# Kernel tuning notes

Measured on AMD Instinct MI355X. Metric: run time of the kernel, lower is better.

## Reference

```python
import jax, jax.numpy as jnp
import numpy as np

N, E, D, H, C, ED = 30000, 300000, 256, 8, 32, 32
HID = H * C  # 256 = hidden_channels


def setup_inputs() -> dict:
    key = jax.random.key(0)
    ks = jax.random.split(key, 14)
    w = lambda k, shp, fan: (jax.random.normal(k, shp, jnp.float32) / np.sqrt(fan)).astype(jnp.float32)
    return {
        "x": jax.random.normal(ks[0], (N, D), jnp.float32),
        "edge_index": jax.random.randint(ks[1], (2, E), 0, N, jnp.int32),
        "edge_attr": jax.random.normal(ks[2], (E, ED), jnp.float32),
        # TransformerConv params (PyG: q/k/v Linears have bias; lin_edge & lin_skip bias=False)
        "Wq": w(ks[3], (D, HID), D), "bq": 0.01 * jax.random.normal(ks[4], (HID,), jnp.float32),
        "Wk": w(ks[5], (D, HID), D), "bk": 0.01 * jax.random.normal(ks[6], (HID,), jnp.float32),
        "Wv": w(ks[7], (D, HID), D), "bv": 0.01 * jax.random.normal(ks[8], (HID,), jnp.float32),
        "We": w(ks[9], (ED, HID), ED),
        "Wskip": w(ks[10], (D, HID), D),
        # MLP([HID, HID, HID], gelu-tanh, plain_last=False): two Linear+act layers
        "W1": w(ks[11], (HID, HID), HID), "b1": jnp.zeros((HID,), jnp.float32),
        "W2": w(ks[12], (HID, HID), HID), "b2": jnp.zeros((HID,), jnp.float32),
    }


def reference(x, edge_index, edge_attr, Wq, bq, Wk, bk, Wv, bv, We, Wskip, W1, b1, W2, b2):
    src, dst = edge_index[0], edge_index[1]  # message flows src -> dst
    q = (x @ Wq + bq).reshape(N, H, C)
    k = (x @ Wk + bk).reshape(N, H, C)
    v = (x @ Wv + bv).reshape(N, H, C)
    e = (edge_attr @ We).reshape(E, H, C)
    k_e = k[src] + e                               # [E,H,C]
    v_e = v[src] + e                               # [E,H,C]
    logits = jnp.einsum('ehc,ehc->eh', q[dst], k_e) / np.sqrt(C)  # [E,H]
    # segment softmax over incoming edges of each dst node
    m = jax.ops.segment_max(logits, dst, num_segments=N)          # [N,H]
    a = jnp.exp(logits - m[dst])
    denom = jax.ops.segment_sum(a, dst, num_segments=N)           # [N,H]
    alpha = a / (denom[dst] + 1e-16)                              # [E,H]
    agg = jax.ops.segment_sum(alpha[:, :, None] * v_e, dst, num_segments=N)  # [N,H,C]
    out = agg.reshape(N, HID) + x @ Wskip          # concat heads + root skip
    # residual MLP: x + gelu(gelu(x W1 + b1) W2 + b2)
    h = jax.nn.gelu(out @ W1 + b1, approximate=True)
    h = jax.nn.gelu(h @ W2 + b2, approximate=True)
    return out + h
```

## Files before the change

### kernel.cpp

```cpp
#include <hip/hip_runtime.h>

#define NN 30000
#define NE 300000
#define HIDDEN 256

typedef __attribute__((ext_vector_type(8))) __bf16 bf16x8;
typedef __attribute__((ext_vector_type(4))) __bf16 bf16x4;
typedef __attribute__((ext_vector_type(4))) float float4v;

__device__ inline __bf16 f2bf(float f) {
  unsigned u = __builtin_bit_cast(unsigned, f);
  u += 0x7fffu + ((u >> 16) & 1u);
  unsigned short s = (unsigned short)(u >> 16);
  return __builtin_bit_cast(__bf16, s);
}
__device__ inline float bf2f(__bf16 b) {
  unsigned short s = __builtin_bit_cast(unsigned short, b);
  unsigned u = ((unsigned)s) << 16;
  return __builtin_bit_cast(float, u);
}
__device__ inline float gelu_tanh(float x) {
  float x3 = x * x * x;
  return 0.5f * x * (1.0f + tanhf(0.79788456080286536f * (x + 0.044715f * x3)));
}

#define PREP_XB_END (1829 + (NN * 32 + 255) / 256)
__global__ __launch_bounds__(256) void prep_kernel(
    const float* __restrict__ Wq, const float* __restrict__ Wk, const float* __restrict__ Wv,
    const float* __restrict__ Wsk, const float* __restrict__ W1, const float* __restrict__ W2,
    const float* __restrict__ We, const float* __restrict__ bq, const float* __restrict__ bk,
    const float* __restrict__ bv, const float* __restrict__ x,
    __bf16* __restrict__ WTall, __bf16* __restrict__ WT1, __bf16* __restrict__ WT2,
    float* __restrict__ ball, float* __restrict__ WeT, __bf16* __restrict__ xb,
    int* __restrict__ degz) {
  const int b = blockIdx.x;
  const int tid = threadIdx.x;
  if (b < 1792) {
    const int region = b >> 8;
    const int idx = ((b & 255) << 8) | tid;
    const int k = idx & 255, n = idx >> 8;
    float v;
    if (region == 3) {
      const int h = n >> 5, d = n & 31;
      const float* wq = Wq + (size_t)k * 256 + h * 32;
      const float* we = We + (size_t)d * 256 + h * 32;
      float s = 0.f;
#pragma unroll
      for (int c = 0; c < 32; ++c) s += wq[c] * we[c];
      v = s;
    } else {
      const float* W = (region == 0) ? Wq : (region == 1) ? Wk : (region == 2) ? Wv
                     : (region == 4) ? Wsk : (region == 5) ? W1 : W2;
      v = W[(size_t)k * 256 + n];
    }
    const __bf16 bv16 = f2bf(v);
    if (region < 5) WTall[(size_t)region * 65536 + idx] = bv16;
    else if (region == 5) WT1[idx] = bv16;
    else WT2[idx] = bv16;
  } else if (b < 1797) {
    const int j = (b - 1792) * 256 + tid;
    if (j < 1280) {
      float v = 0.f;
      if (j < 256) v = bq[j];
      else if (j < 512) v = bk[j - 256];
      else if (j < 768) v = bv[j - 512];
      else if (j < 1024) {
        const int col = j - 768, h = col >> 5, d = col & 31;
        const float* bqh = bq + h * 32;
        const float* we = We + (size_t)d * 256 + h * 32;
        float s = 0.f;
#pragma unroll
        for (int c = 0; c < 32; ++c) s += bqh[c] * we[c];
        v = s;
      }
      ball[j] = v;
    }
  } else if (b < 1829) {
    const int idx = (b - 1797) * 256 + tid;
    const int ch = idx >> 5, d = idx & 31;
    WeT[idx] = We[(size_t)d * 256 + ch];
  } else if (b < PREP_XB_END) {
    const int t = (b - 1829) * 256 + tid;
    if (t < NN * 256 / 8) {
      const float* p = x + (size_t)t * 8;
      float4v f0 = *(const float4v*)(p);
      float4v f1 = *(const float4v*)(p + 4);
      bf16x8 o;
#pragma unroll
      for (int j = 0; j < 4; ++j) { o[j] = f2bf(f0[j]); o[j + 4] = f2bf(f1[j]); }
      *(bf16x8*)(xb + (size_t)t * 8) = o;
    }
  } else {
    const int idx = (b - PREP_XB_END) * 256 + tid;
    if (idx < 2 * NN) degz[idx] = 0;
  }
}

__global__ void count_deg_kernel(const int* __restrict__ dst, int* __restrict__ deg, int E) {
  int e = blockIdx.x * 256 + threadIdx.x;
  if (e < E) atomicAdd(&deg[dst[e]], 1);
}

__global__ __launch_bounds__(256) void deg_psum_kernel(const int* __restrict__ deg,
                                                       int* __restrict__ psum, int n) {
  int i = blockIdx.x * 256 + threadIdx.x;
  int v = (i < n) ? deg[i] : 0;
#pragma unroll
  for (int s = 1; s < 64; s <<= 1) v += __shfl_xor(v, s);
  __shared__ int ws[4];
  if ((threadIdx.x & 63) == 0) ws[threadIdx.x >> 6] = v;
  __syncthreads();
  if (threadIdx.x == 0) psum[blockIdx.x] = ws[0] + ws[1] + ws[2] + ws[3];
}

__global__ __launch_bounds__(128) void psum_scan_kernel(int* __restrict__ psum,
                                                        int* __restrict__ offs, int nb) {
  __shared__ int tmp[128];
  const int t = threadIdx.x;
  int v = (t < nb) ? psum[t] : 0;
  tmp[t] = v;
  __syncthreads();
  for (int s = 1; s < 128; s <<= 1) {
    int u = (t >= s) ? tmp[t - s] : 0;
    __syncthreads();
    tmp[t] += u;
    __syncthreads();
  }
  if (t < nb) psum[t] = tmp[t] - v;
  if (t == 0) offs[NN] = NE;
}

__global__ __launch_bounds__(256) void offs_kernel(const int* __restrict__ deg,
                                                   const int* __restrict__ psum,
                                                   int* __restrict__ offs, int n) {
  __shared__ int tmp[256];
  const int t = threadIdx.x;
  const int i = blockIdx.x * 256 + t;
  int v = (i < n) ? deg[i] : 0;
  tmp[t] = v;
  __syncthreads();
  for (int s = 1; s < 256; s <<= 1) {
    int u = (t >= s) ? tmp[t - s] : 0;
    __syncthreads();
    tmp[t] += u;
    __syncthreads();
  }
  if (i < n) offs[i] = psum[blockIdx.x] + tmp[t] - v;
}

__global__ void scatter_kernel(const int* __restrict__ srcIn, const int* __restrict__ dstIn,
                               const float* __restrict__ ea,
                               const int* __restrict__ offs, int* __restrict__ cursor,
                               int* __restrict__ srcs, __bf16* __restrict__ eaC, int E) {
  int e = blockIdx.x * 256 + threadIdx.x;
  if (e >= E) return;
  const float* src = ea + (size_t)e * 32;
  float4v f[8];
#pragma unroll
  for (int t = 0; t < 8; ++t) f[t] = *(const float4v*)(src + t * 4);
  int d = dstIn[e];
  int p = atomicAdd(&cursor[d], 1);
  int o = offs[d] + p;
  srcs[o] = srcIn[e];
  __bf16* dstp = eaC + (size_t)o * 32;
#pragma unroll
  for (int t = 0; t < 4; ++t) {
    bf16x8 b;
#pragma unroll
    for (int j = 0; j < 4; ++j) { b[j] = f2bf(f[t * 2][j]); b[j + 4] = f2bf(f[t * 2 + 1][j]); }
    *(bf16x8*)(dstp + t * 8) = b;
  }
}

template <int GX, int EPI, int MODE>
__global__ __launch_bounds__(256) void gemm_k4(
    const __bf16* __restrict__ A, const __bf16* __restrict__ Wt,
    const float* __restrict__ bias,
    float* __restrict__ Yf, __bf16* __restrict__ Ybf,
    __bf16* __restrict__ QGp, __bf16* __restrict__ KVp,
    const float* __restrict__ resid, int M, int gyTiles) {
  __shared__ char smem[128 * 264 * 2];
  __bf16* Bs = (__bf16*)smem;
  const int bid = blockIdx.x;
  const int stripe = bid / (8 * GX);
  const int rem = bid % (8 * GX);
  const int y8 = rem % 8;
  const int xt = rem / 8;
  const int y = stripe * 8 + y8;
  if (y >= gyTiles) return;
  const int n0 = xt * 128;

  {
    const int t = threadIdx.x;
#pragma unroll
    for (int i = 0; i < 16; ++i) {
      int g = i * 256 + t;
      int row = g >> 5;
      int c16 = g & 31;
      bf16x8 v = *(const bf16x8*)(Wt + (size_t)(n0 + row) * 256 + c16 * 8);
      *(bf16x8*)(Bs + row * 264 + c16 * 8) = v;
    }
  }
  __syncthreads();

  const int lane = threadIdx.x & 63;
  const int w = threadIdx.x >> 6;
  const int r = lane & 15;
  const int q = lane >> 4;
  const int mw = y * 128 + w * 32;
  int ar0 = mw + r;      if (ar0 >= M) ar0 = M - 1;
  int ar1 = mw + 16 + r; if (ar1 >= M) ar1 = M - 1;
  const int kq = q * 8;

  float4v acc[2][8];
#pragma unroll
  for (int i = 0; i < 2; ++i)
#pragma unroll
    for (int t = 0; t < 8; ++t) acc[i][t] = (float4v){0.f, 0.f, 0.f, 0.f};

#pragma unroll
  for (int kk = 0; kk < 256; kk += 32) {
    const int ka = kk + kq;
    bf16x8 a0 = *(const bf16x8*)(A + (size_t)ar0 * 256 + ka);
    bf16x8 a1 = *(const bf16x8*)(A + (size_t)ar1 * 256 + ka);
    bf16x8 b[8];
#pragma unroll
    for (int t = 0; t < 8; ++t)
      b[t] = *(const bf16x8*)(Bs + (t * 16 + r) * 264 + ka);
#pragma unroll
    for (int t = 0; t < 8; ++t) {
      acc[0][t] = __builtin_amdgcn_mfma_f32_16x16x32_bf16(a0, b[t], acc[0][t], 0, 0, 0);
      acc[1][t] = __builtin_amdgcn_mfma_f32_16x16x32_bf16(a1, b[t], acc[1][t], 0, 0, 0);
    }
  }
  __syncthreads();

  float* cs = (float*)smem + w * 4224;
#pragma unroll
  for (int t = 0; t < 8; ++t) {
    const int col = n0 + t * 16 + r;
    const float bb = bias ? bias[col] : 0.0f;
#pragma unroll
    for (int i2 = 0; i2 < 2; ++i2)
#pragma unroll
      for (int ii = 0; ii < 4; ++ii) {
        float v = acc[i2][t][ii] + bb;
        if constexpr (EPI == 2 || EPI == 3) v = gelu_tanh(v);
        cs[(i2 * 16 + q * 4 + ii) * 132 + t * 16 + r] = v;
      }
  }

  constexpr int NSTR = GX * 128;
  const int p = n0 >> 8;
  const int cbase = n0 & 255;
  __bf16* dstI = (p == 0 || p == 3) ? QGp : KVp;
  const int moff = (p >= 2) ? 4 : 0;
#pragma unroll
  for (int i = 0; i < 16; ++i) {
    const int rl = i * 2 + (lane >> 5);
    const int row = mw + rl;
    const int c4 = (lane & 31) * 4;
    float4v v = *(const float4v*)(cs + rl * 132 + c4);
    if (row < M) {
      if constexpr (MODE == 1) {
        if (p == 4) {
          *(float4v*)(Yf + (size_t)row * 256 + cbase + c4) = v;
        } else {
          bf16x4 b4;
          b4[0] = f2bf(v[0]); b4[1] = f2bf(v[1]); b4[2] = f2bf(v[2]); b4[3] = f2bf(v[3]);
          const int c = cbase + c4;
          *(bf16x4*)(dstI + (size_t)row * 512 + 2 * c + moff) = b4;
        }
      } else if constexpr (EPI == 1) {
        *(float4v*)(Yf + (size_t)row * NSTR + n0 + c4) = v;
      } else if constexpr (EPI == 3) {
        float4v rr = *(const float4v*)(resid + (size_t)row * NSTR + n0 + c4);
        v[0] += rr[0]; v[1] += rr[1]; v[2] += rr[2]; v[3] += rr[3];
        *(float4v*)(Yf + (size_t)row * NSTR + n0 + c4) = v;
      } else {
        bf16x4 b4;
        b4[0] = f2bf(v[0]); b4[1] = f2bf(v[1]); b4[2] = f2bf(v[2]); b4[3] = f2bf(v[3]);
        *(bf16x4*)(Ybf + (size_t)row * NSTR + n0 + c4) = b4;
      }
    }
  }
}

__global__ __launch_bounds__(256) void attn_kernel(
    const __bf16* __restrict__ QG, const __bf16* __restrict__ KV,
    const __bf16* __restrict__ eaC,
    const int* __restrict__ srcs, const int* __restrict__ offs,
    float* __restrict__ OUT, __bf16* __restrict__ AE) {
  __shared__ float sdn[4][64];
  __shared__ float sav[4][64][4], sae[4][64][4];
  const int lane = threadIdx.x & 63;
  const int w = threadIdx.x >> 6;
  const int n = blockIdx.x;
  const int sub = lane & 7;

  const float LSC = 0.25506589858f;
  const bf16x8 qg = *(const bf16x8*)(QG + (size_t)n * 512 + lane * 8);
  const float q0 = bf2f(qg[0]) * LSC, q1 = bf2f(qg[1]) * LSC;
  const float q2 = bf2f(qg[2]) * LSC, q3 = bf2f(qg[3]) * LSC;
  const float g0 = bf2f(qg[4]) * LSC, g1 = bf2f(qg[5]) * LSC;
  const float g2 = bf2f(qg[6]) * LSC, g3 = bf2f(qg[7]) * LSC;

  float denom = 0.f;
  float4v accv = {0.f, 0.f, 0.f, 0.f};
  float4v acce = {0.f, 0.f, 0.f, 0.f};
  const int beg = offs[n], end = offs[n + 1];

  int i = beg + w;
  for (; i + 4 < end; i += 8) {
    const int s0 = srcs[i];
    const int s1 = srcs[i + 4];
    const bf16x8 kv0 = *(const bf16x8*)(KV + (size_t)s0 * 512 + lane * 8);
    const bf16x4 a0 = *(const bf16x4*)(eaC + (size_t)i * 32 + sub * 4);
    const bf16x8 kv1 = *(const bf16x8*)(KV + (size_t)s1 * 512 + lane * 8);
    const bf16x4 a1 = *(const bf16x4*)(eaC + (size_t)(i + 4) * 32 + sub * 4);
    const float e00 = bf2f(a0[0]), e01 = bf2f(a0[1]), e02 = bf2f(a0[2]), e03 = bf2f(a0[3]);
    const float e10 = bf2f(a1[0]), e11 = bf2f(a1[1]), e12 = bf2f(a1[2]), e13 = bf2f(a1[3]);
    float p0 = q0 * bf2f(kv0[0]) + q1 * bf2f(kv0[1]) + q2 * bf2f(kv0[2]) + q3 * bf2f(kv0[3])
             + g0 * e00 + g1 * e01 + g2 * e02 + g3 * e03;
    float p1 = q0 * bf2f(kv1[0]) + q1 * bf2f(kv1[1]) + q2 * bf2f(kv1[2]) + q3 * bf2f(kv1[3])
             + g0 * e10 + g1 * e11 + g2 * e12 + g3 * e13;
    p0 += __shfl_xor(p0, 1); p1 += __shfl_xor(p1, 1);
    p0 += __shfl_xor(p0, 2); p1 += __shfl_xor(p1, 2);
    p0 += __shfl_xor(p0, 4); p1 += __shfl_xor(p1, 4);
    const float w0 = exp2f(p0);
    const float w1 = exp2f(p1);
    denom += w0 + w1;
    accv[0] += w0 * bf2f(kv0[4]) + w1 * bf2f(kv1[4]);
    accv[1] += w0 * bf2f(kv0[5]) + w1 * bf2f(kv1[5]);
    accv[2] += w0 * bf2f(kv0[6]) + w1 * bf2f(kv1[6]);
    accv[3] += w0 * bf2f(kv0[7]) + w1 * bf2f(kv1[7]);
    acce[0] += w0 * e00 + w1 * e10;
    acce[1] += w0 * e01 + w1 * e11;
    acce[2] += w0 * e02 + w1 * e12;
    acce[3] += w0 * e03 + w1 * e13;
  }
  if (i < end) {
    const int s0 = srcs[i];
    const bf16x8 kv0 = *(const bf16x8*)(KV + (size_t)s0 * 512 + lane * 8);
    const bf16x4 a0 = *(const bf16x4*)(eaC + (size_t)i * 32 + sub * 4);
    const float e00 = bf2f(a0[0]), e01 = bf2f(a0[1]), e02 = bf2f(a0[2]), e03 = bf2f(a0[3]);
    float p0 = q0 * bf2f(kv0[0]) + q1 * bf2f(kv0[1]) + q2 * bf2f(kv0[2]) + q3 * bf2f(kv0[3])
             + g0 * e00 + g1 * e01 + g2 * e02 + g3 * e03;
    p0 += __shfl_xor(p0, 1);
    p0 += __shfl_xor(p0, 2);
    p0 += __shfl_xor(p0, 4);
    const float w0 = exp2f(p0);
    denom += w0;
    accv[0] += w0 * bf2f(kv0[4]);
    accv[1] += w0 * bf2f(kv0[5]);
    accv[2] += w0 * bf2f(kv0[6]);
    accv[3] += w0 * bf2f(kv0[7]);
    acce[0] += w0 * e00;
    acce[1] += w0 * e01;
    acce[2] += w0 * e02;
    acce[3] += w0 * e03;
  }

  sdn[w][lane] = denom;
#pragma unroll
  for (int j = 0; j < 4; ++j) { sav[w][lane][j] = accv[j]; sae[w][lane][j] = acce[j]; }
  __syncthreads();
  if (w == 0) {
    float D = 0.f;
    float4v av = {0.f, 0.f, 0.f, 0.f};
    float4v ae = {0.f, 0.f, 0.f, 0.f};
#pragma unroll
    for (int ww = 0; ww < 4; ++ww) {
      D += sdn[ww][lane];
#pragma unroll
      for (int j = 0; j < 4; ++j) { av[j] += sav[ww][lane][j]; ae[j] += sae[ww][lane][j]; }
    }
    const float inv = 1.0f / (D + 1e-16f);
    const int c0 = lane * 4;
    float4v o = *(const float4v*)(OUT + (size_t)n * 256 + c0);
#pragma unroll
    for (int j = 0; j < 4; ++j) o[j] += av[j] * inv;
    *(float4v*)(OUT + (size_t)n * 256 + c0) = o;
    bf16x4 aeb;
    aeb[0] = f2bf(ae[0] * inv); aeb[1] = f2bf(ae[1] * inv);
    aeb[2] = f2bf(ae[2] * inv); aeb[3] = f2bf(ae[3] * inv);
    *(bf16x4*)(AE + (size_t)n * 256 + c0) = aeb;
  }
}

__global__ __launch_bounds__(256) void post_kernel(
    const __bf16* __restrict__ AE, const float* __restrict__ WeT,
    float* __restrict__ OUT, __bf16* __restrict__ OUTh) {
  const int lane = threadIdx.x & 63;
  const int wave = threadIdx.x >> 6;
  const int c0 = lane * 4;
  const int hg = lane >> 3;

  float4v w4[4][8];
#pragma unroll
  for (int j = 0; j < 4; ++j)
#pragma unroll
    for (int s = 0; s < 8; ++s)
      w4[j][s] = *(const float4v*)(WeT + (size_t)(c0 + j) * 32 + s * 4);

  const int nbase = blockIdx.x * 64;
  for (int it = 0; it < 16; ++it) {
    const int n = nbase + it * 4 + wave;
    if (n >= NN) return;
    const __bf16* aerow = AE + (size_t)n * HIDDEN + hg * 32;
    float aef[32];
#pragma unroll
    for (int t = 0; t < 4; ++t) {
      bf16x8 a8 = *(const bf16x8*)(aerow + t * 8);
#pragma unroll
      for (int j = 0; j < 8; ++j) aef[t * 8 + j] = bf2f(a8[j]);
    }
    float4v o = *(const float4v*)(OUT + (size_t)n * HIDDEN + c0);
#pragma unroll
    for (int j = 0; j < 4; ++j) {
      float s = 0.f;
#pragma unroll
      for (int g = 0; g < 8; ++g) {
        s += aef[g * 4 + 0] * w4[j][g][0] + aef[g * 4 + 1] * w4[j][g][1]
           + aef[g * 4 + 2] * w4[j][g][2] + aef[g * 4 + 3] * w4[j][g][3];
      }
      o[j] += s;
    }
    *(float4v*)(OUT + (size_t)n * HIDDEN + c0) = o;
    bf16x4 ob;
    ob[0] = f2bf(o[0]); ob[1] = f2bf(o[1]); ob[2] = f2bf(o[2]); ob[3] = f2bf(o[3]);
    *(bf16x4*)(OUTh + (size_t)n * HIDDEN + c0) = ob;
  }
}

extern "C" void kernel_launch(void* const* d_in, const int* in_sizes, int n_in,
                              void* d_out, int out_size, void* d_ws, size_t ws_size,
                              hipStream_t stream) {
  (void)in_sizes; (void)n_in; (void)out_size; (void)ws_size;
  const float* x   = (const float*)d_in[0];
  const int*   ei  = (const int*)d_in[1];
  const float* ea  = (const float*)d_in[2];
  const float* Wq  = (const float*)d_in[3];
  const float* bq  = (const float*)d_in[4];
  const float* Wk  = (const float*)d_in[5];
  const float* bk  = (const float*)d_in[6];
  const float* Wv  = (const float*)d_in[7];
  const float* bv  = (const float*)d_in[8];
  const float* We  = (const float*)d_in[9];
  const float* Wsk = (const float*)d_in[10];
  const float* W1  = (const float*)d_in[11];
  const float* b1  = (const float*)d_in[12];
  const float* W2  = (const float*)d_in[13];
  const float* b2  = (const float*)d_in[14];
  float* out = (float*)d_out;

  char* ws = (char*)d_ws;
  size_t off = 0;
  auto alloc = [&](size_t bytes) -> char* {
    off = (off + 255) & ~(size_t)255;
    char* p = ws + off;
    off += bytes;
    return p;
  };
  __bf16* QG   = (__bf16*)alloc((size_t)NN * 512 * 2);
  __bf16* KV   = (__bf16*)alloc((size_t)NN * 512 * 2);
  __bf16* xb   = (__bf16*)alloc((size_t)NN * 256 * 2);
  __bf16* AE   = (__bf16*)alloc((size_t)NN * 256 * 2);
  __bf16* OUTh = (__bf16*)alloc((size_t)NN * 256 * 2);
  __bf16* eaC  = (__bf16*)alloc((size_t)NE * 32 * 2);
  __bf16* WTall = (__bf16*)alloc((size_t)1280 * 256 * 2);
  __bf16* WT1  = (__bf16*)alloc(256 * 256 * 2);
  __bf16* WT2  = (__bf16*)alloc(256 * 256 * 2);
  float*  ball = (float*)alloc(1280 * 4);
  float*  WeT  = (float*)alloc(256 * 32 * 4);
  int* deg    = (int*)alloc((size_t)2 * NN * 4);
  int* cursor = deg + NN;
  int* offs   = (int*)alloc((size_t)(NN + 1) * 4);
  int* psum   = (int*)alloc(512);
  int* srcs   = (int*)alloc((size_t)NE * 4);
  __bf16* H1 = AE;

  const int* srcIn = ei;
  const int* dstIn = ei + NE;

  const int prepBlocks = PREP_XB_END + (2 * NN + 255) / 256;
  prep_kernel<<<prepBlocks, 256, 0, stream>>>(Wq, Wk, Wv, Wsk, W1, W2, We, bq, bk, bv, x,
                                              WTall, WT1, WT2, ball, WeT, xb, deg);

  const int nb = (NN + 255) / 256;
  count_deg_kernel<<<(NE + 255) / 256, 256, 0, stream>>>(dstIn, deg, NE);
  deg_psum_kernel<<<nb, 256, 0, stream>>>(deg, psum, NN);
  psum_scan_kernel<<<1, 128, 0, stream>>>(psum, offs, nb);
  offs_kernel<<<nb, 256, 0, stream>>>(deg, psum, offs, NN);
  scatter_kernel<<<(NE + 255) / 256, 256, 0, stream>>>(srcIn, dstIn, ea, offs, cursor,
                                                       srcs, eaC, NE);

  const int gy = (NN + 127) / 128;
  const int stripes = (gy + 7) / 8;
  gemm_k4<10, 0, 1><<<stripes * 80, 256, 0, stream>>>(
      xb, WTall, ball, out, nullptr, QG, KV, nullptr, NN, gy);

  attn_kernel<<<NN, 256, 0, stream>>>(QG, KV, eaC, srcs, offs, out, AE);

  post_kernel<<<(NN + 63) / 64, 256, 0, stream>>>(AE, WeT, out, OUTh);

  gemm_k4<2, 2, 0><<<stripes * 16, 256, 0, stream>>>(
      OUTh, WT1, b1, nullptr, H1, nullptr, nullptr, nullptr, NN, gy);
  gemm_k4<2, 3, 0><<<stripes * 16, 256, 0, stream>>>(
      H1, WT2, b2, out, nullptr, nullptr, nullptr, out, NN, gy);
}
```

Measured before the change: 354.7 us.

## Fuse CSR offset scan into one kernel and batch source index loads in attention

Replaces the three-kernel degree prefix sum with a single kernel where each block recomputes its base offset by summing all preceding degrees. In the attention kernel, each wave loads 64 source indices at once and broadcasts them with readlane. The final reduction is spread across all four waves instead of only wave 0. The aim is to cut launch overhead and the serial index-load latency, at the cost of redundant degree reads in later scan blocks.

```diff
diff --git a/kernel.cpp b/kernel.cpp
--- a/kernel.cpp
+++ b/kernel.cpp
@@ -101,51 +101,30 @@
   if (e < E) atomicAdd(&deg[dst[e]], 1);
 }
 
-__global__ __launch_bounds__(256) void deg_psum_kernel(const int* __restrict__ deg,
-                                                       int* __restrict__ psum, int n) {
-  int i = blockIdx.x * 256 + threadIdx.x;
-  int v = (i < n) ? deg[i] : 0;
-#pragma unroll
-  for (int s = 1; s < 64; s <<= 1) v += __shfl_xor(v, s);
-  __shared__ int ws[4];
-  if ((threadIdx.x & 63) == 0) ws[threadIdx.x >> 6] = v;
-  __syncthreads();
-  if (threadIdx.x == 0) psum[blockIdx.x] = ws[0] + ws[1] + ws[2] + ws[3];
-}
-
-__global__ __launch_bounds__(128) void psum_scan_kernel(int* __restrict__ psum,
-                                                        int* __restrict__ offs, int nb) {
-  __shared__ int tmp[128];
+__global__ __launch_bounds__(256) void offs_fused_kernel(const int* __restrict__ deg,
+                                                         int* __restrict__ offs, int n) {
+  __shared__ int tmp[256];
+  __shared__ int sbase[4];
   const int t = threadIdx.x;
-  int v = (t < nb) ? psum[t] : 0;
-  tmp[t] = v;
-  __syncthreads();
-  for (int s = 1; s < 128; s <<= 1) {
-    int u = (t >= s) ? tmp[t - s] : 0;
-    __syncthreads();
-    tmp[t] += u;
-    __syncthreads();
-  }
-  if (t < nb) psum[t] = tmp[t] - v;
-  if (t == 0) offs[NN] = NE;
-}
-
-__global__ __launch_bounds__(256) void offs_kernel(const int* __restrict__ deg,
-                                                   const int* __restrict__ psum,
-                                                   int* __restrict__ offs, int n) {
-  __shared__ int tmp[256];
-  const int t = threadIdx.x;
-  const int i = blockIdx.x * 256 + t;
+  const int lim = blockIdx.x * 256;
+  int bp = 0;
+  for (int idx = t; idx < lim; idx += 256) bp += deg[idx];
+#pragma unroll
+  for (int s = 1; s < 64; s <<= 1) bp += __shfl_xor(bp, s);
+  if ((t & 63) == 0) sbase[t >> 6] = bp;
+  const int i = lim + t;
   int v = (i < n) ? deg[i] : 0;
   tmp[t] = v;
   __syncthreads();
+  const int base = sbase[0] + sbase[1] + sbase[2] + sbase[3];
   for (int s = 1; s < 256; s <<= 1) {
     int u = (t >= s) ? tmp[t - s] : 0;
     __syncthreads();
     tmp[t] += u;
     __syncthreads();
   }
-  if (i < n) offs[i] = psum[blockIdx.x] + tmp[t] - v;
+  if (i < n) offs[i] = base + tmp[t] - v;
+  if (blockIdx.x == gridDim.x - 1 && t == 0) offs[n] = NE;
 }
 
 __global__ void scatter_kernel(const int* __restrict__ srcIn, const int* __restrict__ dstIn,
@@ -297,6 +276,10 @@
   const int w = threadIdx.x >> 6;
   const int n = blockIdx.x;
   const int sub = lane & 7;
+  const int ch = w * 64 + lane;
+
+  const int beg = offs[n], end = offs[n + 1];
+  const float opre = OUT[(size_t)n * 256 + ch];
 
   const float LSC = 0.25506589858f;
   const bf16x8 qg = *(const bf16x8*)(QG + (size_t)n * 512 + lane * 8);
@@ -308,84 +291,77 @@
   float denom = 0.f;
   float4v accv = {0.f, 0.f, 0.f, 0.f};
   float4v acce = {0.f, 0.f, 0.f, 0.f};
-  const int beg = offs[n], end = offs[n + 1];
-
-  int i = beg + w;
-  for (; i + 4 < end; i += 8) {
-    const int s0 = srcs[i];
-    const int s1 = srcs[i + 4];
-    const bf16x8 kv0 = *(const bf16x8*)(KV + (size_t)s0 * 512 + lane * 8);
-    const bf16x4 a0 = *(const bf16x4*)(eaC + (size_t)i * 32 + sub * 4);
-    const bf16x8 kv1 = *(const bf16x8*)(KV + (size_t)s1 * 512 + lane * 8);
-    const bf16x4 a1 = *(const bf16x4*)(eaC + (size_t)(i + 4) * 32 + sub * 4);
-    const float e00 = bf2f(a0[0]), e01 = bf2f(a0[1]), e02 = bf2f(a0[2]), e03 = bf2f(a0[3]);
-    const float e10 = bf2f(a1[0]), e11 = bf2f(a1[1]), e12 = bf2f(a1[2]), e13 = bf2f(a1[3]);
-    float p0 = q0 * bf2f(kv0[0]) + q1 * bf2f(kv0[1]) + q2 * bf2f(kv0[2]) + q3 * bf2f(kv0[3])
-             + g0 * e00 + g1 * e01 + g2 * e02 + g3 * e03;
-    float p1 = q0 * bf2f(kv1[0]) + q1 * bf2f(kv1[1]) + q2 * bf2f(kv1[2]) + q3 * bf2f(kv1[3])
-             + g0 * e10 + g1 * e11 + g2 * e12 + g3 * e13;
-    p0 += __shfl_xor(p0, 1); p1 += __shfl_xor(p1, 1);
-    p0 += __shfl_xor(p0, 2); p1 += __shfl_xor(p1, 2);
-    p0 += __shfl_xor(p0, 4); p1 += __shfl_xor(p1, 4);
-    const float w0 = exp2f(p0);
-    const float w1 = exp2f(p1);
-    denom += w0 + w1;
-    accv[0] += w0 * bf2f(kv0[4]) + w1 * bf2f(kv1[4]);
-    accv[1] += w0 * bf2f(kv0[5]) + w1 * bf2f(kv1[5]);
-    accv[2] += w0 * bf2f(kv0[6]) + w1 * bf2f(kv1[6]);
-    accv[3] += w0 * bf2f(kv0[7]) + w1 * bf2f(kv1[7]);
-    acce[0] += w0 * e00 + w1 * e10;
-    acce[1] += w0 * e01 + w1 * e11;
-    acce[2] += w0 * e02 + w1 * e12;
-    acce[3] += w0 * e03 + w1 * e13;
-  }
-  if (i < end) {
-    const int s0 = srcs[i];
-    const bf16x8 kv0 = *(const bf16x8*)(KV + (size_t)s0 * 512 + lane * 8);
-    const bf16x4 a0 = *(const bf16x4*)(eaC + (size_t)i * 32 + sub * 4);
-    const float e00 = bf2f(a0[0]), e01 = bf2f(a0[1]), e02 = bf2f(a0[2]), e03 = bf2f(a0[3]);
-    float p0 = q0 * bf2f(kv0[0]) + q1 * bf2f(kv0[1]) + q2 * bf2f(kv0[2]) + q3 * bf2f(kv0[3])
-             + g0 * e00 + g1 * e01 + g2 * e02 + g3 * e03;
-    p0 += __shfl_xor(p0, 1);
-    p0 += __shfl_xor(p0, 2);
-    p0 += __shfl_xor(p0, 4);
-    const float w0 = exp2f(p0);
-    denom += w0;
-    accv[0] += w0 * bf2f(kv0[4]);
-    accv[1] += w0 * bf2f(kv0[5]);
-    accv[2] += w0 * bf2f(kv0[6]);
-    accv[3] += w0 * bf2f(kv0[7]);
-    acce[0] += w0 * e00;
-    acce[1] += w0 * e01;
-    acce[2] += w0 * e02;
-    acce[3] += w0 * e03;
+
+  for (int b0 = beg; b0 < end; b0 += 64) {
+    const int rem = end - b0;
+    const int cnt = (rem < 64) ? rem : 64;
+    const int sl = (lane < cnt) ? lane : cnt - 1;
+    const int myS = srcs[b0 + sl];
+
+    int j = w;
+    for (; j + 4 < cnt; j += 8) {
+      const int s0 = __builtin_amdgcn_readlane(myS, j);
+      const int s1 = __builtin_amdgcn_readlane(myS, j + 4);
+      const bf16x8 kv0 = *(const bf16x8*)(KV + (size_t)s0 * 512 + lane * 8);
+      const bf16x4 a0 = *(const bf16x4*)(eaC + (size_t)(b0 + j) * 32 + sub * 4);
+      const bf16x8 kv1 = *(const bf16x8*)(KV + (size_t)s1 * 512 + lane * 8);
+      const bf16x4 a1 = *(const bf16x4*)(eaC + (size_t)(b0 + j + 4) * 32 + sub * 4);
+      const float e00 = bf2f(a0[0]), e01 = bf2f(a0[1]), e02 = bf2f(a0[2]), e03 = bf2f(a0[3]);
+      const float e10 = bf2f(a1[0]), e11 = bf2f(a1[1]), e12 = bf2f(a1[2]), e13 = bf2f(a1[3]);
+      float p0 = q0 * bf2f(kv0[0]) + q1 * bf2f(kv0[1]) + q2 * bf2f(kv0[2]) + q3 * bf2f(kv0[3])
+               + g0 * e00 + g1 * e01 + g2 * e02 + g3 * e03;
+      float p1 = q0 * bf2f(kv1[0]) + q1 * bf2f(kv1[1]) + q2 * bf2f(kv1[2]) + q3 * bf2f(kv1[3])
+               + g0 * e10 + g1 * e11 + g2 * e12 + g3 * e13;
+      p0 += __shfl_xor(p0, 1); p1 += __shfl_xor(p1, 1);
+      p0 += __shfl_xor(p0, 2); p1 += __shfl_xor(p1, 2);
+      p0 += __shfl_xor(p0, 4); p1 += __shfl_xor(p1, 4);
+      const float w0 = exp2f(p0);
+      const float w1 = exp2f(p1);
+      denom += w0 + w1;
+      accv[0] += w0 * bf2f(kv0[4]) + w1 * bf2f(kv1[4]);
+      accv[1] += w0 * bf2f(kv0[5]) + w1 * bf2f(kv1[5]);
+      accv[2] += w0 * bf2f(kv0[6]) + w1 * bf2f(kv1[6]);
+      accv[3] += w0 * bf2f(kv0[7]) + w1 * bf2f(kv1[7]);
+      acce[0] += w0 * e00 + w1 * e10;
+      acce[1] += w0 * e01 + w1 * e11;
+      acce[2] += w0 * e02 + w1 * e12;
+      acce[3] += w0 * e03 + w1 * e13;
+    }
+    if (j < cnt) {
+      const int s0 = __builtin_amdgcn_readlane(myS, j);
+      const bf16x8 kv0 = *(const bf16x8*)(KV + (size_t)s0 * 512 + lane * 8);
+      const bf16x4 a0 = *(const bf16x4*)(eaC + (size_t)(b0 + j) * 32 + sub * 4);
+      const float e00 = bf2f(a0[0]), e01 = bf2f(a0[1]), e02 = bf2f(a0[2]), e03 = bf2f(a0[3]);
+      float p0 = q0 * bf2f(kv0[0]) + q1 * bf2f(kv0[1]) + q2 * bf2f(kv0[2]) + q3 * bf2f(kv0[3])
+               + g0 * e00 + g1 * e01 + g2 * e02 + g3 * e03;
+      p0 += __shfl_xor(p0, 1);
+      p0 += __shfl_xor(p0, 2);
+      p0 += __shfl_xor(p0, 4);
+      const float w0 = exp2f(p0);
+      denom += w0;
+      accv[0] += w0 * bf2f(kv0[4]);
+      accv[1] += w0 * bf2f(kv0[5]);
+      accv[2] += w0 * bf2f(kv0[6]);
+      accv[3] += w0 * bf2f(kv0[7]);
+      acce[0] += w0 * e00;
+      acce[1] += w0 * e01;
+      acce[2] += w0 * e02;
+      acce[3] += w0 * e03;
+    }
   }
 
   sdn[w][lane] = denom;
 #pragma unroll
   for (int j = 0; j < 4; ++j) { sav[w][lane][j] = accv[j]; sae[w][lane][j] = acce[j]; }
   __syncthreads();
-  if (w == 0) {
-    float D = 0.f;
-    float4v av = {0.f, 0.f, 0.f, 0.f};
-    float4v ae = {0.f, 0.f, 0.f, 0.f};
-#pragma unroll
-    for (int ww = 0; ww < 4; ++ww) {
-      D += sdn[ww][lane];
-#pragma unroll
-      for (int j = 0; j < 4; ++j) { av[j] += sav[ww][lane][j]; ae[j] += sae[ww][lane][j]; }
-    }
-    const float inv = 1.0f / (D + 1e-16f);
-    const int c0 = lane * 4;
-    float4v o = *(const float4v*)(OUT + (size_t)n * 256 + c0);
-#pragma unroll
-    for (int j = 0; j < 4; ++j) o[j] += av[j] * inv;
-    *(float4v*)(OUT + (size_t)n * 256 + c0) = o;
-    bf16x4 aeb;
-    aeb[0] = f2bf(ae[0] * inv); aeb[1] = f2bf(ae[1] * inv);
-    aeb[2] = f2bf(ae[2] * inv); aeb[3] = f2bf(ae[3] * inv);
-    *(bf16x4*)(AE + (size_t)n * 256 + c0) = aeb;
-  }
+
+  const int lp = ch >> 2, jp = ch & 3;
+  const float D = sdn[0][lp] + sdn[1][lp] + sdn[2][lp] + sdn[3][lp];
+  const float av = sav[0][lp][jp] + sav[1][lp][jp] + sav[2][lp][jp] + sav[3][lp][jp];
+  const float ae = sae[0][lp][jp] + sae[1][lp][jp] + sae[2][lp][jp] + sae[3][lp][jp];
+  const float inv = 1.0f / (D + 1e-16f);
+  OUT[(size_t)n * 256 + ch] = opre + av * inv;
+  AE[(size_t)n * 256 + ch] = f2bf(ae * inv);
 }
 
 __global__ __launch_bounds__(256) void post_kernel(
@@ -476,7 +452,6 @@
   int* deg    = (int*)alloc((size_t)2 * NN * 4);
   int* cursor = deg + NN;
   int* offs   = (int*)alloc((size_t)(NN + 1) * 4);
-  int* psum   = (int*)alloc(512);
   int* srcs   = (int*)alloc((size_t)NE * 4);
   __bf16* H1 = AE;
 
@@ -489,9 +464,7 @@
 
   const int nb = (NN + 255) / 256;
   count_deg_kernel<<<(NE + 255) / 256, 256, 0, stream>>>(dstIn, deg, NE);
-  deg_psum_kernel<<<nb, 256, 0, stream>>>(deg, psum, NN);
-  psum_scan_kernel<<<1, 128, 0, stream>>>(psum, offs, nb);
-  offs_kernel<<<nb, 256, 0, stream>>>(deg, psum, offs, NN);
+  offs_fused_kernel<<<nb, 256, 0, stream>>>(deg, offs, NN);
   scatter_kernel<<<(NE + 255) / 256, 256, 0, stream>>>(srcIn, dstIn, ea, offs, cursor,
                                                        srcs, eaC, NE);
 
```

Result: slower. 368.6 us (+3.9%).
